# Performance work log

Measured on AMD Instinct MI355X. Metric: run time of the kernel, lower is better.

## Reference

```python
import jax, jax.numpy as jnp
import numpy as np

BS, N, H, F_IN, F_OUT = 4, 2048, 2, 768, 768
NEG_SLOPE = 0.2

def setup_inputs() -> dict:
    key = jax.random.key(0)
    k_h, k_adj, k_w, k_as, k_ad = jax.random.split(key, 5)
    h = jax.random.normal(k_h, (BS, N, F_IN), dtype=jnp.float32)
    adj = jax.random.randint(k_adj, (BS, N, N), 0, 2) > 0  # bool adjacency
    # xavier_uniform fan_in/fan_out per torch semantics on [H, f_in, f_out]
    limit_w = float(np.sqrt(6.0 / (F_IN + F_OUT)))
    w = jax.random.uniform(k_w, (H, F_IN, F_OUT), minval=-limit_w, maxval=limit_w, dtype=jnp.float32)
    limit_a = float(np.sqrt(6.0 / (F_OUT + 1)))
    a_src = jax.random.uniform(k_as, (H, F_OUT, 1), minval=-limit_a, maxval=limit_a, dtype=jnp.float32)
    a_dst = jax.random.uniform(k_ad, (H, F_OUT, 1), minval=-limit_a, maxval=limit_a, dtype=jnp.float32)
    bias = jnp.zeros((F_OUT,), dtype=jnp.float32)
    return {"h": h, "adj": adj, "w": w, "a_src": a_src, "a_dst": a_dst, "bias": bias}

def reference(h, adj, w, a_src, a_dst, bias):
    # h: [b, n, f_in]; w: [H, f_in, f_out] -> h_prime: [b, H, n, f_out]
    h_prime = jnp.einsum('bnf,hfo->bhno', h, w)
    t = jnp.tanh(h_prime)
    attn_src = jnp.einsum('bhno,ho->bhn', t, a_src[..., 0])  # [b, H, n]
    attn_dst = jnp.einsum('bhno,ho->bhn', t, a_dst[..., 0])  # [b, H, n]
    # broadcast add: scores[b,h,i,j] = src[i] + dst[j]
    attn = attn_src[:, :, :, None] + attn_dst[:, :, None, :]
    attn = jnp.where(attn >= 0, attn, NEG_SLOPE * attn)  # leaky_relu
    n = adj.shape[-1]
    keep = adj[:, None, :, :] | jnp.eye(n, dtype=bool)[None, None]  # [b,1,n,n]
    attn = jnp.where(keep, attn, -jnp.inf)
    attn = jax.nn.softmax(attn, axis=-1)
    # dropout is identity at inference
    out = jnp.einsum('bhij,bhjo->bhio', attn, h_prime)
    return out + bias
```

## Files before the change

kernel.cpp:

```cpp
#include <hip/hip_runtime.h>
#include <hip/hip_bf16.h>
#include <cstdint>
#include <cstddef>

#define BS   4
#define NN   2048
#define NH   2
#define FIN  768
#define FOUT 768
#define NEG_SLOPE 0.2f

typedef __attribute__((ext_vector_type(8))) short short8;
typedef __attribute__((ext_vector_type(4))) float float4v;

static __device__ __forceinline__ float bits2f(unsigned short u) {
    union { unsigned int i; float f; } v; v.i = ((unsigned int)u) << 16; return v.f;
}
static __device__ __forceinline__ unsigned short f2bits(float f) {
    union { float f; unsigned int i; } v; v.f = f;
    unsigned int x = v.i;
    unsigned int r = x + 0x7fffu + ((x >> 16) & 1u);
    return (unsigned short)(r >> 16);
}
static __device__ __forceinline__ float fast_tanh(float x) {
    float xc = fminf(fmaxf(x, -20.f), 20.f);
    float e = __expf(2.f * xc);
    return (e - 1.f) / (e + 1.f);
}
static __device__ __forceinline__ void async_copy16(void* lds, const void* g) {
    __builtin_amdgcn_global_load_lds(
        (const __attribute__((address_space(1))) unsigned int*)g,
        (__attribute__((address_space(3))) unsigned int*)lds, 16, 0, 0);
}

static __device__ __forceinline__ bool detect_isf32(const unsigned short* h_raw) {
    unsigned short u = h_raw[threadIdx.x & 63];
    int e = (u >> 7) & 0xFF;
    unsigned long long m = __ballot(e >= 118 && e <= 134);
    return __popcll(m) < 48;
}
static __device__ __forceinline__ bool detect_adj8(const unsigned char* adj_raw) {
    int l = threadIdx.x & 63;
    unsigned char v = (unsigned char)(adj_raw[l * 4 + 1] | adj_raw[l * 4 + 2] |
                                      adj_raw[l * 4 + 3]);
    unsigned long long m = __ballot(v != 0);
    return __popcll(m) > 8;
}

#define NB_H   3072
#define NB_W   1152
#define NB_Z   128
__global__ __launch_bounds__(256) void k_prep(
    const void* __restrict__ hr, unsigned short* __restrict__ h_bf,
    const void* __restrict__ wr, unsigned short* __restrict__ wt_b,
    const void* __restrict__ as_raw, const void* __restrict__ ad_raw,
    const void* __restrict__ b_raw,
    float* __restrict__ asf, float* __restrict__ adf, float* __restrict__ bff,
    float* __restrict__ attn_acc)
{
    __shared__ float tile[32][33];
    int bi = blockIdx.x;
    int t = threadIdx.x;
    if (bi < NB_H) {
        bool isf = detect_isf32((const unsigned short*)hr);
        int base = (bi * 256 + t) * 8;
        if (isf) {
            float4 f0 = *((const float4*)((const float*)hr + base));
            float4 f1 = *((const float4*)((const float*)hr + base + 4));
            unsigned short v[8] = { f2bits(f0.x), f2bits(f0.y), f2bits(f0.z), f2bits(f0.w),
                                    f2bits(f1.x), f2bits(f1.y), f2bits(f1.z), f2bits(f1.w) };
            *(uint4*)(h_bf + base) = *(const uint4*)v;
        } else {
            *(uint4*)(h_bf + base) = *(const uint4*)((const unsigned short*)hr + base);
        }
        return;
    }
    if (bi < NB_H + NB_W) {
        bool isf = detect_isf32((const unsigned short*)hr);
        int wb = bi - NB_H;
        int h  = wb / 576;
        int rem = wb % 576;
        int f0 = (rem % 24) * 32;
        int o0 = (rem / 24) * 32;
        int tx = t & 31, ty = t >> 5;
        #pragma unroll
        for (int r = 0; r < 4; ++r) {
            int fl = ty * 4 + r;
            size_t idx = (size_t)h * FIN * FOUT + (size_t)(f0 + fl) * FOUT + (o0 + tx);
            tile[fl][tx] = isf ? ((const float*)wr)[idx]
                               : bits2f(((const unsigned short*)wr)[idx]);
        }
        __syncthreads();
        #pragma unroll
        for (int r = 0; r < 4; ++r) {
            int ol = ty * 4 + r;
            size_t oidx = (size_t)h * FOUT * FIN + (size_t)(o0 + ol) * FIN + (f0 + tx);
            wt_b[oidx] = f2bits(tile[tx][ol]);
        }
        return;
    }
    if (bi < NB_H + NB_W + NB_Z) {
        attn_acc[(bi - NB_H - NB_W) * 256 + t] = 0.f;
        return;
    }
    bool isf = detect_isf32((const unsigned short*)hr);
    for (int i = t; i < NH * FOUT; i += 256) {
        asf[i] = isf ? ((const float*)as_raw)[i] : bits2f(((const unsigned short*)as_raw)[i]);
        adf[i] = isf ? ((const float*)ad_raw)[i] : bits2f(((const unsigned short*)ad_raw)[i]);
    }
    for (int i = t; i < FOUT; i += 256)
        bff[i] = isf ? ((const float*)b_raw)[i] : bits2f(((const unsigned short*)b_raw)[i]);
}

#define BM 128
#define BN 128
#define BK 64

__global__ __launch_bounds__(256) void k_gemm_hw(
    const unsigned short* __restrict__ hh,
    const unsigned short* __restrict__ wh,
    unsigned short* __restrict__ hpT,
    const float* __restrict__ asf, const float* __restrict__ adf,
    float* __restrict__ attn_src, float* __restrict__ attn_dst)
{
    int ib = blockIdx.z;
    int b  = ib / NH, hd = ib % NH;
    int i0 = blockIdx.x * BM;
    int o0 = blockIdx.y * BN;
    const unsigned short* A  = hh + (size_t)b  * NN * FIN;
    const unsigned short* Bt = wh + (size_t)hd * FOUT * FIN;
    unsigned short*       C  = hpT + (size_t)ib * FOUT * NN;

    __shared__ __align__(16) unsigned short As[BM * BK];
    __shared__ __align__(16) unsigned short Bs[BN * BK];

    int t = threadIdx.x;
    int lane = t & 63, wave = t >> 6;
    int wm = (wave & 1) * 64, wn = (wave >> 1) * 64;
    int lm = lane & 15, quad = lane >> 4;
    int rr = lane >> 3;
    int cc = lane & 7;
    int gc = cc ^ rr;
    int e  = lm & 7;

    float4v acc[4][4] = {};

    for (int k0 = 0; k0 < FIN; k0 += BK) {
        __syncthreads();
        #pragma unroll
        for (int p = 0; p < 4; ++p) {
            int r0 = wave * 32 + p * 8;
            async_copy16(&As[r0 * BK], A  + (size_t)(i0 + r0 + rr) * FIN + k0 + gc * 8);
            async_copy16(&Bs[r0 * BK], Bt + (size_t)(o0 + r0 + rr) * FIN + k0 + gc * 8);
        }
        __syncthreads();
        #pragma unroll
        for (int kk = 0; kk < 2; ++kk) {
            int slot = ((kk << 2) | quad) ^ e;
            short8 fa[4], fb[4];
            #pragma unroll
            for (int mt = 0; mt < 4; ++mt)
                fa[mt] = *(const short8*)&As[(wm + mt * 16 + lm) * BK + slot * 8];
            #pragma unroll
            for (int nt = 0; nt < 4; ++nt)
                fb[nt] = *(const short8*)&Bs[(wn + nt * 16 + lm) * BK + slot * 8];
            #pragma unroll
            for (int mt = 0; mt < 4; ++mt)
                #pragma unroll
                for (int nt = 0; nt < 4; ++nt)
                    acc[mt][nt] = __builtin_amdgcn_mfma_f32_16x16x32_bf16(
                        fa[mt], fb[nt], acc[mt][nt], 0, 0, 0);
        }
    }

    float asv[4], adv[4];
    #pragma unroll
    for (int nt = 0; nt < 4; ++nt) {
        int o = o0 + wn + nt * 16 + lm;
        asv[nt] = asf[hd * FOUT + o];
        adv[nt] = adf[hd * FOUT + o];
    }
    #pragma unroll
    for (int mt = 0; mt < 4; ++mt) {
        float ps[4] = {0.f, 0.f, 0.f, 0.f};
        float pd[4] = {0.f, 0.f, 0.f, 0.f};
        #pragma unroll
        for (int nt = 0; nt < 4; ++nt) {
            int node = i0 + wm + mt * 16 + quad * 4;
            int o    = o0 + wn + nt * 16 + lm;
            ushort4 v;
            v.x = f2bits(acc[mt][nt][0]);
            v.y = f2bits(acc[mt][nt][1]);
            v.z = f2bits(acc[mt][nt][2]);
            v.w = f2bits(acc[mt][nt][3]);
            *(ushort4*)&C[(size_t)o * NN + node] = v;
            #pragma unroll
            for (int r = 0; r < 4; ++r) {
                float tv = fast_tanh(acc[mt][nt][r]);
                ps[r] += tv * asv[nt];
                pd[r] += tv * adv[nt];
            }
        }
        #pragma unroll
        for (int r = 0; r < 4; ++r) {
            float s = ps[r], d = pd[r];
            #pragma unroll
            for (int off = 1; off <= 8; off <<= 1) {
                s += __shfl_xor(s, off);
                d += __shfl_xor(d, off);
            }
            if (lm == 0) {
                int node = i0 + wm + mt * 16 + quad * 4 + r;
                atomicAdd(&attn_src[ib * NN + node], s);
                atomicAdd(&attn_dst[ib * NN + node], d);
            }
        }
    }
}

__global__ __launch_bounds__(256) void k_softmax_p(
    const float* __restrict__ attn_src, const float* __restrict__ attn_dst,
    const void* __restrict__ adj_raw,
    unsigned short* __restrict__ P)
{
    int blk = blockIdx.x;
    int i = blk & (NN - 1);
    int b = blk >> 11;
    bool is8 = detect_adj8((const unsigned char*)adj_raw);
    int t = threadIdx.x;
    int lane = t & 63, wave = t >> 6;
    int j0 = t * 8;

    bool keep[8];
    if (is8) {
        const unsigned char* arow = (const unsigned char*)adj_raw + ((size_t)b * NN + i) * NN;
        uint2 v = *(const uint2*)(arow + j0);
        #pragma unroll
        for (int r = 0; r < 8; ++r) {
            unsigned int w = (r < 4) ? v.x : v.y;
            keep[r] = ((w >> ((r & 3) * 8)) & 0xFFu) != 0;
        }
    } else {
        const int* arow = (const int*)adj_raw + ((size_t)b * NN + i) * NN;
        int4 v0 = *(const int4*)(arow + j0);
        int4 v1 = *(const int4*)(arow + j0 + 4);
        keep[0] = v0.x != 0; keep[1] = v0.y != 0; keep[2] = v0.z != 0; keep[3] = v0.w != 0;
        keep[4] = v1.x != 0; keep[5] = v1.y != 0; keep[6] = v1.z != 0; keep[7] = v1.w != 0;
    }
    #pragma unroll
    for (int r = 0; r < 8; ++r) keep[r] = keep[r] || (j0 + r == i);

    __shared__ float redm[4], reds[4];
    for (int hh = 0; hh < NH; ++hh) {
        int bh = b * NH + hh;
        float src = attn_src[bh * NN + i];
        const float* drow = attn_dst + (size_t)bh * NN;
        float4 d0 = *(const float4*)(drow + j0);
        float4 d1 = *(const float4*)(drow + j0 + 4);
        float dj[8] = { d0.x, d0.y, d0.z, d0.w, d1.x, d1.y, d1.z, d1.w };

        float s[8];
        float lmax = -1e30f;
        #pragma unroll
        for (int r = 0; r < 8; ++r) {
            float sc = src + dj[r];
            sc = sc >= 0.f ? sc : NEG_SLOPE * sc;
            s[r] = keep[r] ? sc : -1e30f;
            lmax = fmaxf(lmax, s[r]);
        }
        __syncthreads();
        #pragma unroll
        for (int off = 32; off > 0; off >>= 1)
            lmax = fmaxf(lmax, __shfl_xor(lmax, off));
        if (lane == 0) redm[wave] = lmax;
        __syncthreads();
        float m = fmaxf(fmaxf(redm[0], redm[1]), fmaxf(redm[2], redm[3]));

        float p[8];
        float lsum = 0.f;
        #pragma unroll
        for (int r = 0; r < 8; ++r) {
            p[r] = __expf(s[r] - m);
            lsum += p[r];
        }
        #pragma unroll
        for (int off = 32; off > 0; off >>= 1)
            lsum += __shfl_xor(lsum, off);
        if (lane == 0) reds[wave] = lsum;
        __syncthreads();
        float inv = 1.0f / (reds[0] + reds[1] + reds[2] + reds[3]);

        uint4 pw;
        pw.x = ((unsigned int)f2bits(p[1] * inv) << 16) | f2bits(p[0] * inv);
        pw.y = ((unsigned int)f2bits(p[3] * inv) << 16) | f2bits(p[2] * inv);
        pw.z = ((unsigned int)f2bits(p[5] * inv) << 16) | f2bits(p[4] * inv);
        pw.w = ((unsigned int)f2bits(p[7] * inv) << 16) | f2bits(p[6] * inv);
        *(uint4*)&P[((size_t)bh * NN + i) * NN + j0] = pw;
    }
}

__global__ __launch_bounds__(256) void k_gemm_out(
    const unsigned short* __restrict__ P,
    const unsigned short* __restrict__ hpT,
    const float* __restrict__ bf,
    void* __restrict__ outp, const unsigned short* __restrict__ h_raw)
{
    bool isf = detect_isf32(h_raw);
    int ib = blockIdx.z;
    int i0 = blockIdx.x * BM;
    int o0 = blockIdx.y * BN;
    const unsigned short* A  = P   + (size_t)ib * NN * NN;
    const unsigned short* Bt = hpT + (size_t)ib * FOUT * NN;

    __shared__ __align__(16) unsigned short As[BM * BK];
    __shared__ __align__(16) unsigned short Bs[BN * BK];

    int t = threadIdx.x;
    int lane = t & 63, wave = t >> 6;
    int wm = (wave & 1) * 64, wn = (wave >> 1) * 64;
    int lm = lane & 15, quad = lane >> 4;
    int rr = lane >> 3;
    int cc = lane & 7;
    int gc = cc ^ rr;
    int e  = lm & 7;

    float4v acc[4][4] = {};

    for (int k0 = 0; k0 < NN; k0 += BK) {
        __syncthreads();
        #pragma unroll
        for (int p = 0; p < 4; ++p) {
            int r0 = wave * 32 + p * 8;
            async_copy16(&As[r0 * BK], A  + (size_t)(i0 + r0 + rr) * NN + k0 + gc * 8);
            async_copy16(&Bs[r0 * BK], Bt + (size_t)(o0 + r0 + rr) * NN + k0 + gc * 8);
        }
        __syncthreads();
        #pragma unroll
        for (int kk = 0; kk < 2; ++kk) {
            int slot = ((kk << 2) | quad) ^ e;
            short8 fa[4], fb[4];
            #pragma unroll
            for (int mt = 0; mt < 4; ++mt)
                fa[mt] = *(const short8*)&As[(wm + mt * 16 + lm) * BK + slot * 8];
            #pragma unroll
            for (int nt = 0; nt < 4; ++nt)
                fb[nt] = *(const short8*)&Bs[(wn + nt * 16 + lm) * BK + slot * 8];
            #pragma unroll
            for (int mt = 0; mt < 4; ++mt)
                #pragma unroll
                for (int nt = 0; nt < 4; ++nt)
                    acc[mt][nt] = __builtin_amdgcn_mfma_f32_16x16x32_bf16(
                        fa[mt], fb[nt], acc[mt][nt], 0, 0, 0);
        }
    }

    if (isf) {
        float* C = (float*)outp + (size_t)ib * NN * FOUT;
        #pragma unroll
        for (int nt = 0; nt < 4; ++nt) {
            int o = o0 + wn + nt * 16 + lm;
            float bv = bf[o];
            #pragma unroll
            for (int mt = 0; mt < 4; ++mt) {
                int i = i0 + wm + mt * 16 + quad * 4;
                #pragma unroll
                for (int r = 0; r < 4; ++r)
                    C[(size_t)(i + r) * FOUT + o] = acc[mt][nt][r] + bv;
            }
        }
    } else {
        unsigned short* C = (unsigned short*)outp + (size_t)ib * NN * FOUT;
        #pragma unroll
        for (int nt = 0; nt < 4; ++nt) {
            int o = o0 + wn + nt * 16 + lm;
            float bv = bf[o];
            #pragma unroll
            for (int mt = 0; mt < 4; ++mt) {
                int i = i0 + wm + mt * 16 + quad * 4;
                #pragma unroll
                for (int r = 0; r < 4; ++r)
                    C[(size_t)(i + r) * FOUT + o] = f2bits(acc[mt][nt][r] + bv);
            }
        }
    }
}

extern "C" void kernel_launch(void* const* d_in, const int* in_sizes, int n_in,
                              void* d_out, int out_size, void* d_ws, size_t ws_size,
                              hipStream_t stream)
{
    const void* h_raw   = d_in[0];
    const void* adj_raw = d_in[1];
    const void* w_raw   = d_in[2];
    const void* as_raw  = d_in[3];
    const void* ad_raw  = d_in[4];
    const void* b_raw   = d_in[5];

    char* ws = (char*)d_ws;
    size_t off = 0;
    unsigned short* hpT = (unsigned short*)(ws + off); off += (size_t)BS * NH * FOUT * NN * 2;
    float* asr = (float*)(ws + off);            off += (size_t)BS * NH * NN * 4;
    float* ads = (float*)(ws + off);            off += (size_t)BS * NH * NN * 4;
    size_t uoff = off;
    unsigned short* P    = (unsigned short*)(ws + uoff);
    unsigned short* h_bf = (unsigned short*)(ws + uoff); uoff += (size_t)BS * NN * FIN * 2;
    unsigned short* wt_b = (unsigned short*)(ws + uoff); uoff += (size_t)NH * FOUT * FIN * 2;
    off += (size_t)BS * NH * NN * NN * 2;
    float* asf = (float*)(ws + off);            off += (size_t)NH * FOUT * 4;
    float* adf = (float*)(ws + off);            off += (size_t)NH * FOUT * 4;
    float* bff = (float*)(ws + off);            off += 4096;

    k_prep<<<NB_H + NB_W + NB_Z + 1, 256, 0, stream>>>(
        h_raw, h_bf, w_raw, wt_b, as_raw, ad_raw, b_raw, asf, adf, bff, asr);
    k_gemm_hw<<<dim3(NN / BM, FOUT / BN, BS * NH), 256, 0, stream>>>(
        h_bf, wt_b, hpT, asf, adf, asr, ads);
    k_softmax_p<<<dim3(BS * NN), 256, 0, stream>>>(asr, ads, adj_raw, P);
    k_gemm_out<<<dim3(NN / BM, FOUT / BN, BS * NH), 256, 0, stream>>>(
        P, hpT, bff, d_out, (const unsigned short*)h_raw);
}
```

Before: 280.8 us.

## Fuse softmax probability generation into output GEMM using adjacency bitmask

Replaces the materialized bf16 probability matrix P (BS*NH*N*N, about 67MB) with a packed adjacency bitmask plus per-row max and inverse-sum statistics. The output GEMM recomputes the probabilities on the fly from attn_src, attn_dst, the bitmask and the row stats, writing them into a padded LDS tile instead of async-copying P. This removes the large P write and read traffic. The cost is redundant exp/leaky-relu work, since each output-column block regenerates the same tile, and a synchronous compute phase before each MFMA step.

```diff
diff --git a/kernel.cpp b/kernel.cpp
--- a/kernel.cpp
+++ b/kernel.cpp
@@ -218,10 +218,11 @@
     }
 }
 
-__global__ __launch_bounds__(256) void k_softmax_p(
+__global__ __launch_bounds__(256) void k_adjstat(
     const float* __restrict__ attn_src, const float* __restrict__ attn_dst,
     const void* __restrict__ adj_raw,
-    unsigned short* __restrict__ P)
+    unsigned char* __restrict__ bitmask,
+    float* __restrict__ marr, float* __restrict__ ilarr)
 {
     int blk = blockIdx.x;
     int i = blk & (NN - 1);
@@ -250,6 +251,11 @@
     #pragma unroll
     for (int r = 0; r < 8; ++r) keep[r] = keep[r] || (j0 + r == i);
 
+    unsigned int byte = 0;
+    #pragma unroll
+    for (int r = 0; r < 8; ++r) byte |= (keep[r] ? 1u : 0u) << r;
+    bitmask[(size_t)blk * (NN / 8) + t] = (unsigned char)byte;
+
     __shared__ float redm[4], reds[4];
     for (int hh = 0; hh < NH; ++hh) {
         int bh = b * NH + hh;
@@ -276,43 +282,39 @@
         __syncthreads();
         float m = fmaxf(fmaxf(redm[0], redm[1]), fmaxf(redm[2], redm[3]));
 
-        float p[8];
         float lsum = 0.f;
         #pragma unroll
-        for (int r = 0; r < 8; ++r) {
-            p[r] = __expf(s[r] - m);
-            lsum += p[r];
-        }
+        for (int r = 0; r < 8; ++r) lsum += __expf(s[r] - m);
         #pragma unroll
         for (int off = 32; off > 0; off >>= 1)
             lsum += __shfl_xor(lsum, off);
         if (lane == 0) reds[wave] = lsum;
         __syncthreads();
-        float inv = 1.0f / (reds[0] + reds[1] + reds[2] + reds[3]);
-
-        uint4 pw;
-        pw.x = ((unsigned int)f2bits(p[1] * inv) << 16) | f2bits(p[0] * inv);
-        pw.y = ((unsigned int)f2bits(p[3] * inv) << 16) | f2bits(p[2] * inv);
-        pw.z = ((unsigned int)f2bits(p[5] * inv) << 16) | f2bits(p[4] * inv);
-        pw.w = ((unsigned int)f2bits(p[7] * inv) << 16) | f2bits(p[6] * inv);
-        *(uint4*)&P[((size_t)bh * NN + i) * NN + j0] = pw;
-    }
-}
-
+        if (t == 0) {
+            float l = reds[0] + reds[1] + reds[2] + reds[3];
+            marr[bh * NN + i]  = m;
+            ilarr[bh * NN + i] = 1.0f / l;
+        }
+    }
+}
+
+#define ASTR 72
 __global__ __launch_bounds__(256) void k_gemm_out(
-    const unsigned short* __restrict__ P,
+    const unsigned char* __restrict__ bitmask,
+    const float* __restrict__ attn_src, const float* __restrict__ attn_dst,
+    const float* __restrict__ marr, const float* __restrict__ ilarr,
     const unsigned short* __restrict__ hpT,
     const float* __restrict__ bf,
     void* __restrict__ outp, const unsigned short* __restrict__ h_raw)
 {
     bool isf = detect_isf32(h_raw);
     int ib = blockIdx.z;
+    int b  = ib / NH;
     int i0 = blockIdx.x * BM;
     int o0 = blockIdx.y * BN;
-    const unsigned short* A  = P   + (size_t)ib * NN * NN;
     const unsigned short* Bt = hpT + (size_t)ib * FOUT * NN;
 
-    __shared__ __align__(16) unsigned short As[BM * BK];
+    __shared__ __align__(16) unsigned short As[BM * ASTR];
     __shared__ __align__(16) unsigned short Bs[BN * BK];
 
     int t = threadIdx.x;
@@ -324,6 +326,14 @@
     int gc = cc ^ rr;
     int e  = lm & 7;
 
+    int ia = t >> 1;
+    int jh = (t & 1) * 32;
+    float src_i = attn_src[ib * NN + i0 + ia];
+    float m_i   = marr[ib * NN + i0 + ia];
+    float il_i  = ilarr[ib * NN + i0 + ia];
+    const unsigned char* mrow = bitmask + ((size_t)b * NN + i0 + ia) * (NN / 8);
+    const float* dstv = attn_dst + (size_t)ib * NN;
+
     float4v acc[4][4] = {};
 
     for (int k0 = 0; k0 < NN; k0 += BK) {
@@ -331,20 +341,36 @@
         #pragma unroll
         for (int p = 0; p < 4; ++p) {
             int r0 = wave * 32 + p * 8;
-            async_copy16(&As[r0 * BK], A  + (size_t)(i0 + r0 + rr) * NN + k0 + gc * 8);
             async_copy16(&Bs[r0 * BK], Bt + (size_t)(o0 + r0 + rr) * NN + k0 + gc * 8);
         }
+        #pragma unroll
+        for (int g = 0; g < 4; ++g) {
+            int j = k0 + jh + g * 8;
+            unsigned int m8 = mrow[j >> 3];
+            float4 d0 = *(const float4*)(dstv + j);
+            float4 d1 = *(const float4*)(dstv + j + 4);
+            float dj[8] = { d0.x, d0.y, d0.z, d0.w, d1.x, d1.y, d1.z, d1.w };
+            unsigned short v[8];
+            #pragma unroll
+            for (int r = 0; r < 8; ++r) {
+                float tt = src_i + dj[r];
+                float lr = fmaxf(tt, 0.f) + NEG_SLOPE * fminf(tt, 0.f);
+                float arg = ((m8 >> r) & 1u) ? (lr - m_i) : -1e30f;
+                v[r] = f2bits(__expf(arg) * il_i);
+            }
+            *(uint4*)&As[ia * ASTR + jh + g * 8] = *(const uint4*)v;
+        }
         __syncthreads();
         #pragma unroll
         for (int kk = 0; kk < 2; ++kk) {
-            int slot = ((kk << 2) | quad) ^ e;
+            int slotB = ((kk << 2) | quad) ^ e;
             short8 fa[4], fb[4];
             #pragma unroll
             for (int mt = 0; mt < 4; ++mt)
-                fa[mt] = *(const short8*)&As[(wm + mt * 16 + lm) * BK + slot * 8];
+                fa[mt] = *(const short8*)&As[(wm + mt * 16 + lm) * ASTR + kk * 32 + quad * 8];
             #pragma unroll
             for (int nt = 0; nt < 4; ++nt)
-                fb[nt] = *(const short8*)&Bs[(wn + nt * 16 + lm) * BK + slot * 8];
+                fb[nt] = *(const short8*)&Bs[(wn + nt * 16 + lm) * BK + slotB * 8];
             #pragma unroll
             for (int mt = 0; mt < 4; ++mt)
                 #pragma unroll
@@ -399,13 +425,13 @@
     char* ws = (char*)d_ws;
     size_t off = 0;
     unsigned short* hpT = (unsigned short*)(ws + off); off += (size_t)BS * NH * FOUT * NN * 2;
-    float* asr = (float*)(ws + off);            off += (size_t)BS * NH * NN * 4;
-    float* ads = (float*)(ws + off);            off += (size_t)BS * NH * NN * 4;
-    size_t uoff = off;
-    unsigned short* P    = (unsigned short*)(ws + uoff);
-    unsigned short* h_bf = (unsigned short*)(ws + uoff); uoff += (size_t)BS * NN * FIN * 2;
-    unsigned short* wt_b = (unsigned short*)(ws + uoff); uoff += (size_t)NH * FOUT * FIN * 2;
-    off += (size_t)BS * NH * NN * NN * 2;
+    float* asr  = (float*)(ws + off);           off += (size_t)BS * NH * NN * 4;
+    float* ads  = (float*)(ws + off);           off += (size_t)BS * NH * NN * 4;
+    float* marr = (float*)(ws + off);           off += (size_t)BS * NH * NN * 4;
+    float* ilar = (float*)(ws + off);           off += (size_t)BS * NH * NN * 4;
+    unsigned short* h_bf = (unsigned short*)(ws + off); off += (size_t)BS * NN * FIN * 2;
+    unsigned short* wt_b = (unsigned short*)(ws + off); off += (size_t)NH * FOUT * FIN * 2;
+    unsigned char* bmask = (unsigned char*)(ws + off);  off += (size_t)BS * NN * (NN / 8);
     float* asf = (float*)(ws + off);            off += (size_t)NH * FOUT * 4;
     float* adf = (float*)(ws + off);            off += (size_t)NH * FOUT * 4;
     float* bff = (float*)(ws + off);            off += 4096;
@@ -414,7 +440,7 @@
         h_raw, h_bf, w_raw, wt_b, as_raw, ad_raw, b_raw, asf, adf, bff, asr);
     k_gemm_hw<<<dim3(NN / BM, FOUT / BN, BS * NH), 256, 0, stream>>>(
         h_bf, wt_b, hpT, asf, adf, asr, ads);
-    k_softmax_p<<<dim3(BS * NN), 256, 0, stream>>>(asr, ads, adj_raw, P);
+    k_adjstat<<<dim3(BS * NN), 256, 0, stream>>>(asr, ads, adj_raw, bmask, marr, ilar);
     k_gemm_out<<<dim3(NN / BM, FOUT / BN, BS * NH), 256, 0, stream>>>(
-        P, hpT, bff, d_out, (const unsigned short*)h_raw);
-}
+        bmask, asr, ads, marr, ilar, hpT, bff, d_out, (const unsigned short*)h_raw);
+}
```

Measured after the change: 352.3 us. 25.5% more time.
